# Performance work log

Hardware: AMD Instinct MI355X
Metric: run time of the kernel (lower is better)

## Reference

```python
import jax, jax.numpy as jnp
import numpy as np

B, L, D, H = 4, 1024, 1024, 16
DH = D // H
NEG = -1e9
EPS = 1e-5


def setup_inputs() -> dict:
    key = jax.random.key(0)
    ks = jax.random.split(key, 12)
    s = 1.0 / np.sqrt(D)
    inp = {
        "Q": jax.random.normal(ks[0], (B, L, D), jnp.float32),
        "K": jax.random.normal(ks[1], (B, L, D), jnp.float32),
        "V": jax.random.normal(ks[2], (B, L, D), jnp.float32),
        "K_mask": jnp.ones((B, L), jnp.int32),
        "WQ": jax.random.normal(ks[3], (D, D), jnp.float32) * s,
        "bQ": jnp.zeros((D,), jnp.float32),
        "WK": jax.random.normal(ks[4], (D, D), jnp.float32) * s,
        "bK": jnp.zeros((D,), jnp.float32),
        "WV": jax.random.normal(ks[5], (D, D), jnp.float32) * s,
        "bV": jnp.zeros((D,), jnp.float32),
        "WO": jax.random.normal(ks[6], (D, D), jnp.float32) * s,
        "bO": jnp.zeros((D,), jnp.float32),
        "ln_g": jnp.ones((D,), jnp.float32),
        "ln_b": jnp.zeros((D,), jnp.float32),
    }
    return inp


def _mha(Q, K, V, K_mask, WQ, bQ, WK, bK, WV, bV, WO, bO, ln_g, ln_b):
    # projections  [B,L,D]
    q = Q @ WQ + bQ
    k = K @ WK + bK
    v = V @ WV + bV
    # split heads -> [B,H,L,dh]
    q = q.reshape(B, L, H, DH).transpose(0, 2, 1, 3)
    k = k.reshape(B, L, H, DH).transpose(0, 2, 1, 3)
    v = v.reshape(B, L, H, DH).transpose(0, 2, 1, 3)
    # scaled dot product, masked softmax over keys
    scores = jnp.einsum("bhqd,bhkd->bhqk", q, k) / jnp.sqrt(jnp.float32(DH))
    mask = (K_mask > 0)[:, None, None, :]  # [B,1,1,Lk]
    scores = jnp.where(mask, scores, NEG)
    attn = jax.nn.softmax(scores, axis=-1)  # dropout is identity at inference
    ctx = jnp.einsum("bhqk,bhkd->bhqd", attn, v)
    ctx = ctx.transpose(0, 2, 1, 3).reshape(B, L, D)
    # output layer: dense + residual + layernorm
    out = ctx @ WO + bO
    x = out + Q
    mu = jnp.mean(x, axis=-1, keepdims=True)
    var = jnp.var(x, axis=-1, keepdims=True)
    return (x - mu) * jax.lax.rsqrt(var + EPS) * ln_g + ln_b


def reference(Q, K, V, K_mask, WQ, bQ, WK, bK, WV, bV, WO, bO, ln_g, ln_b):
    return _mha(Q, K, V, K_mask, WQ, bQ, WK, bK, WV, bV, WO, bO, ln_g, ln_b)
```

## Files before the change

kernel.cpp:

```cpp
#include <hip/hip_runtime.h>
#include <hip/hip_bf16.h>
#include <stdint.h>

#define Bn 4
#define Ln 1024
#define Dn 1024
#define Hn 16
#define DHn 64
#define Mn (Bn*Ln)

typedef __attribute__((ext_vector_type(8))) short short8v;
typedef __attribute__((ext_vector_type(4))) float floatx4;

__device__ __forceinline__ unsigned short f2b(float f){
  union { float f; unsigned u; } v; v.f = f;
  unsigned r = (v.u + 0x7FFFu + ((v.u >> 16) & 1u)) >> 16;
  return (unsigned short)r;
}
__device__ __forceinline__ unsigned short f2b_fast(float f){
  __hip_bfloat16 h = __float2bfloat16(f);
  return *reinterpret_cast<unsigned short*>(&h);
}
__device__ __forceinline__ float b2f(unsigned short u){
  union { unsigned u; float f; } v; v.u = (unsigned)u << 16; return v.f;
}

typedef const unsigned __attribute__((address_space(1)))* gas1_t;
typedef unsigned __attribute__((address_space(3)))* las3_t;
__device__ __forceinline__ void gload16(const void* g, void* l){
  __builtin_amdgcn_global_load_lds((gas1_t)(uintptr_t)g, (las3_t)(uintptr_t)l, 16, 0, 0);
}

__global__ __launch_bounds__(256) void prep_k(const float* __restrict__ W0,
    const float* __restrict__ W1, const float* __restrict__ W2,
    const float* __restrict__ W3, unsigned short* __restrict__ Wt0,
    unsigned short* __restrict__ Wt1, unsigned short* __restrict__ Wt2,
    unsigned short* __restrict__ Wt3, const float* __restrict__ x0,
    const float* __restrict__ x1, const float* __restrict__ x2,
    unsigned short* __restrict__ o0, unsigned short* __restrict__ o1,
    unsigned short* __restrict__ o2)
{
  __shared__ float tile[64][65];
  if (blockIdx.x < 1024){
    const int z = blockIdx.x >> 8, rem = blockIdx.x & 255;
    const float* W; unsigned short* Wt;
    switch (z){
      case 0: W = W0; Wt = Wt0; break;
      case 1: W = W1; Wt = Wt1; break;
      case 2: W = W2; Wt = Wt2; break;
      default: W = W3; Wt = Wt3; break;
    }
    const int nb = (rem & 15) * 64, kb = (rem >> 4) * 64;
    const int tx = threadIdx.x & 63, ty = threadIdx.x >> 6;
    #pragma unroll
    for (int r = 0; r < 64; r += 4)
      tile[r + ty][tx] = W[(size_t)(kb + r + ty) * 1024 + nb + tx];
    __syncthreads();
    #pragma unroll
    for (int r = 0; r < 64; r += 4)
      Wt[(size_t)(nb + r + ty) * 1024 + kb + tx] = f2b(tile[tx][r + ty]);
  } else {
    const int i = (blockIdx.x - 1024) * 256 + threadIdx.x;
    const int sel = i >> 20, idx = i & 0xFFFFF;
    const float* x = sel == 0 ? x0 : (sel == 1 ? x1 : x2);
    unsigned short* o = sel == 0 ? o0 : (sel == 1 ? o1 : o2);
    float4 v = reinterpret_cast<const float4*>(x)[idx];
    union { unsigned short u[4]; uint2 q; } p;
    p.u[0] = f2b(v.x); p.u[1] = f2b(v.y); p.u[2] = f2b(v.z); p.u[3] = f2b(v.w);
    reinterpret_cast<uint2*>(o)[idx] = p.q;
  }
}

template<int MODE>
__device__ __forceinline__ void gemm8_core(const unsigned short* __restrict__ Ab,
    const unsigned short* __restrict__ Btp, const float* __restrict__ bias,
    void* __restrict__ outp, float scale, unsigned short* lds, int nt, int mt)
{
  const int tid = threadIdx.x;
  const int lane = tid & 63, wave = tid >> 6;
  const int wr = wave >> 2, wc = wave & 3;
  const int lg = lane >> 4, lr = lane & 15;
  const int m0 = mt * 256, n0 = nt * 256;

  const unsigned short* gAb[2];
  const unsigned short* gBb[2];
  int ldso[2];
  #pragma unroll
  for (int i = 0; i < 2; i++){
    int c = tid + 512 * i;
    int g16 = c >> 6, lrr = c & 15, lgg = (c >> 4) & 3;
    int row = g16 * 16 + lrr;
    gAb[i] = Ab  + (size_t)(m0 + row) * 1024 + lgg * 8;
    gBb[i] = Btp + (size_t)(n0 + row) * 1024 + lgg * 8;
    ldso[i] = c * 8;
  }
  auto stageA = [&](int sg){
    unsigned short* slot = lds + (sg & 3) * 16384;
    const int kcol = (sg >> 1) * 64 + (sg & 1) * 32;
    #pragma unroll
    for (int i = 0; i < 2; i++) gload16(gAb[i] + kcol, &slot[ldso[i]]);
  };
  auto stageB = [&](int sg){
    unsigned short* slot = lds + (sg & 3) * 16384 + 8192;
    const int kcol = (sg >> 1) * 64 + (sg & 1) * 32;
    #pragma unroll
    for (int i = 0; i < 2; i++) gload16(gBb[i] + kcol, &slot[ldso[i]]);
  };

  floatx4 acc[8][4] = {};

  stageA(0); stageB(0); stageA(1); stageB(1); stageA(2); stageB(2);

  for (int t = 0; t < 16; t++){
    unsigned short* slot0 = lds + ((2 * t) & 3) * 16384;
    unsigned short* slot1 = lds + ((2 * t + 1) & 3) * 16384;
    short8v af[4], bf[4];
    if (t < 15) asm volatile("s_waitcnt vmcnt(8)" ::: "memory");
    else        asm volatile("s_waitcnt vmcnt(4)" ::: "memory");
    __builtin_amdgcn_s_barrier();
    __builtin_amdgcn_sched_barrier(0);
    if (t < 15) stageA(2 * t + 3);
    #pragma unroll
    for (int n = 0; n < 4; n++)
      bf[n] = *reinterpret_cast<const short8v*>(&slot0[8192 + ((wc * 4 + n) * 64 + lane) * 8]);
    #pragma unroll
    for (int i2 = 0; i2 < 4; i2++)
      af[i2] = *reinterpret_cast<const short8v*>(&slot0[((wr * 8 + i2) * 64 + lane) * 8]);
    __builtin_amdgcn_s_setprio(1);
    #pragma unroll
    for (int a = 0; a < 4; a++)
      #pragma unroll
      for (int n = 0; n < 4; n++)
        acc[a][n] = __builtin_amdgcn_mfma_f32_16x16x32_bf16(af[a], bf[n], acc[a][n], 0, 0, 0);
    __builtin_amdgcn_s_setprio(0);
    if (t < 15) stageB(2 * t + 3);
    #pragma unroll
    for (int i2 = 0; i2 < 4; i2++)
      af[i2] = *reinterpret_cast<const short8v*>(&slot0[((wr * 8 + 4 + i2) * 64 + lane) * 8]);
    __builtin_amdgcn_s_setprio(1);
    #pragma unroll
    for (int a = 0; a < 4; a++)
      #pragma unroll
      for (int n = 0; n < 4; n++)
        acc[4 + a][n] = __builtin_amdgcn_mfma_f32_16x16x32_bf16(af[a], bf[n], acc[4 + a][n], 0, 0, 0);
    __builtin_amdgcn_s_setprio(0);
    __builtin_amdgcn_sched_barrier(0);
    if (t < 15) asm volatile("s_waitcnt vmcnt(8)" ::: "memory");
    else        asm volatile("s_waitcnt vmcnt(0)" ::: "memory");
    __builtin_amdgcn_s_barrier();
    __builtin_amdgcn_sched_barrier(0);
    if (t < 14) stageA(2 * t + 4);
    #pragma unroll
    for (int n = 0; n < 4; n++)
      bf[n] = *reinterpret_cast<const short8v*>(&slot1[8192 + ((wc * 4 + n) * 64 + lane) * 8]);
    #pragma unroll
    for (int i2 = 0; i2 < 4; i2++)
      af[i2] = *reinterpret_cast<const short8v*>(&slot1[((wr * 8 + i2) * 64 + lane) * 8]);
    __builtin_amdgcn_s_setprio(1);
    #pragma unroll
    for (int a = 0; a < 4; a++)
      #pragma unroll
      for (int n = 0; n < 4; n++)
        acc[a][n] = __builtin_amdgcn_mfma_f32_16x16x32_bf16(af[a], bf[n], acc[a][n], 0, 0, 0);
    __builtin_amdgcn_s_setprio(0);
    if (t < 14) stageB(2 * t + 4);
    #pragma unroll
    for (int i2 = 0; i2 < 4; i2++)
      af[i2] = *reinterpret_cast<const short8v*>(&slot1[((wr * 8 + 4 + i2) * 64 + lane) * 8]);
    __builtin_amdgcn_s_setprio(1);
    #pragma unroll
    for (int a = 0; a < 4; a++)
      #pragma unroll
      for (int n = 0; n < 4; n++)
        acc[4 + a][n] = __builtin_amdgcn_mfma_f32_16x16x32_bf16(af[a], bf[n], acc[4 + a][n], 0, 0, 0);
    __builtin_amdgcn_s_setprio(0);
    __builtin_amdgcn_sched_barrier(0);
  }

  if constexpr (MODE == 2){
    __syncthreads();
    #pragma unroll
    for (int n = 0; n < 4; n++){
      const int gn_l = wc * 64 + n * 16 + lr;
      const float bb = bias[n0 + gn_l];
      const int X = (gn_l & 7) << 3;
      #pragma unroll
      for (int a = 0; a < 8; a++){
        const int gm_l = wr * 128 + a * 16 + lg * 4;
        union { unsigned short u[4]; uint2 q; } pk;
        #pragma unroll
        for (int r = 0; r < 4; r++) pk.u[r] = f2b((acc[a][n][r] + bb) * scale);
        *reinterpret_cast<uint2*>(&lds[gn_l * 256 + (gm_l ^ X)]) = pk.q;
      }
    }
    __syncthreads();
    const int bb2 = m0 >> 10, l0 = m0 & 1023;
    const int row = tid >> 1, colb = (tid & 1) * 128;
    const int h2 = (n0 + row) >> 6, d = (n0 + row) & 63;
    unsigned short* obase = (unsigned short*)outp +
        (((size_t)(bb2 * Hn + h2)) * DHn + d) * Ln + l0 + colb;
    const int XR = (row & 7) << 3;
    #pragma unroll
    for (int g = 0; g < 16; g++){
      short8v v = *reinterpret_cast<const short8v*>(&lds[row * 256 + ((colb + g * 8) ^ XR)]);
      *reinterpret_cast<short8v*>(obase + g * 8) = v;
    }
  } else {
    unsigned short* plw = lds + wave * 1152;
    unsigned short* o = (unsigned short*)outp;
    const int gnb = n0 + wc * 64;
    const int h2 = gnb >> 6;
    float bb4[4];
    #pragma unroll
    for (int n = 0; n < 4; n++) bb4[n] = bias[gnb + n * 16 + lr];
    #pragma unroll
    for (int a = 0; a < 8; a++){
      #pragma unroll
      for (int n = 0; n < 4; n++)
        #pragma unroll
        for (int r = 0; r < 4; r++)
          plw[(lg * 4 + r) * 72 + n * 16 + lr] = f2b((acc[a][n][r] + bb4[n]) * scale);
      #pragma unroll
      for (int it = 0; it < 2; it++){
        const int row = it * 8 + (lane >> 3);
        const int c   = lane & 7;
        const int gm  = m0 + wr * 128 + a * 16 + row;
        const int b2 = gm >> 10, l = gm & 1023;
        short8v v = *reinterpret_cast<const short8v*>(&plw[row * 72 + c * 8]);
        *reinterpret_cast<short8v*>(o + (((size_t)(b2 * Hn + h2)) * Ln + l) * DHn + c * 8) = v;
      }
    }
  }
}

__global__ __launch_bounds__(512, 2) void gemmqkv8_k(
    const unsigned short* __restrict__ A0, const unsigned short* __restrict__ A1,
    const unsigned short* __restrict__ A2, const unsigned short* __restrict__ W0,
    const unsigned short* __restrict__ W1, const unsigned short* __restrict__ W2,
    const float* __restrict__ b0, const float* __restrict__ b1,
    const float* __restrict__ b2, unsigned short* __restrict__ o0,
    unsigned short* __restrict__ o1, unsigned short* __restrict__ o2, float qscl)
{
  __shared__ __align__(16) unsigned short lds[65536];
  const int g = blockIdx.x >> 3;
  const int nt = g & 3;
  const int panel = (g >> 2) * 8 + (blockIdx.x & 7);
  const int z = panel >> 4, mt = panel & 15;
  if (z == 0)
    gemm8_core<0>(A0, W0, b0, o0, qscl, lds, nt, mt);
  else if (z == 1)
    gemm8_core<0>(A1, W1, b1, o1, 1.f, lds, nt, mt);
  else
    gemm8_core<2>(A2, W2, b2, o2, 1.f, lds, nt, mt);
}

__global__ __launch_bounds__(256) void gemmo_k(const unsigned short* __restrict__ Ab,
    const unsigned short* __restrict__ W, const float* __restrict__ bias,
    unsigned short* __restrict__ out, const float* __restrict__ resid)
{
  __shared__ __align__(16) unsigned short lds[32768];
  const int bid = blockIdx.x;
  const int xcd = bid & 7, k = bid >> 3;
  const int mt = xcd * 4 + (k >> 3);
  const int nt = k & 7;

  const int tid = threadIdx.x;
  const int lane = tid & 63, wave = tid >> 6;
  const int wr = wave >> 1, wc = wave & 1;
  const int lg = lane >> 4, lr = lane & 15;
  const int m0 = mt * 128, n0 = nt * 128;

  const unsigned short* gA[2];
  const unsigned short* gB[2];
  int ldso[2];
  #pragma unroll
  for (int i = 0; i < 2; i++){
    int c = tid + 256 * i;
    int g16 = c >> 6, lrr = c & 15, lgg = (c >> 4) & 3;
    int row = g16 * 16 + lrr;
    gA[i] = Ab + (size_t)(m0 + row) * 1024 + lgg * 8;
    gB[i] = W  + (size_t)(n0 + row) * 1024 + lgg * 8;
    ldso[i] = c * 8;
  }
  auto issue = [&](int s){
    unsigned short* base = lds + (s & 3) * 8192;
    const int kc = s * 32;
    #pragma unroll
    for (int i = 0; i < 2; i++) gload16(gA[i] + kc, &base[ldso[i]]);
    #pragma unroll
    for (int i = 0; i < 2; i++) gload16(gB[i] + kc, &base[4096 + ldso[i]]);
  };

  floatx4 acc[4][4] = {};

  issue(0); issue(1); issue(2);

  for (int s = 0; s < 32; s++){
    unsigned short* base = lds + (s & 3) * 8192;
    if (s <= 29)      asm volatile("s_waitcnt vmcnt(8)" ::: "memory");
    else if (s == 30) asm volatile("s_waitcnt vmcnt(4)" ::: "memory");
    else              asm volatile("s_waitcnt vmcnt(0)" ::: "memory");
    __builtin_amdgcn_s_barrier();
    __builtin_amdgcn_sched_barrier(0);
    if (s <= 28) issue(s + 3);
    short8v af[4], bf[4];
    #pragma unroll
    for (int m = 0; m < 4; m++)
      af[m] = *reinterpret_cast<const short8v*>(&base[((wr * 4 + m) * 64 + lane) * 8]);
    #pragma unroll
    for (int n = 0; n < 4; n++)
      bf[n] = *reinterpret_cast<const short8v*>(&base[4096 + ((wc * 4 + n) * 64 + lane) * 8]);
    __builtin_amdgcn_s_setprio(1);
    #pragma unroll
    for (int m = 0; m < 4; m++)
      #pragma unroll
      for (int n = 0; n < 4; n++)
        acc[m][n] = __builtin_amdgcn_mfma_f32_16x16x32_bf16(af[m], bf[n], acc[m][n], 0, 0, 0);
    __builtin_amdgcn_s_setprio(0);
    __builtin_amdgcn_sched_barrier(0);
  }

  unsigned short* plw = lds + wave * 1152;
  float bb4[4];
  #pragma unroll
  for (int n = 0; n < 4; n++) bb4[n] = bias[n0 + wc * 64 + n * 16 + lr];
  #pragma unroll
  for (int m = 0; m < 4; m++){
    #pragma unroll
    for (int n = 0; n < 4; n++){
      const int gn = n0 + wc * 64 + n * 16 + lr;
      #pragma unroll
      for (int r = 0; r < 4; r++){
        const int gm = m0 + wr * 64 + m * 16 + lg * 4 + r;
        float v = acc[m][n][r] + bb4[n] + resid[(size_t)gm * Dn + gn];
        plw[(lg * 4 + r) * 72 + n * 16 + lr] = f2b_fast(v);
      }
    }
    #pragma unroll
    for (int it = 0; it < 2; it++){
      const int row = it * 8 + (lane >> 3);
      const int c = lane & 7;
      const int gm = m0 + wr * 64 + m * 16 + row;
      short8v v = *reinterpret_cast<const short8v*>(&plw[row * 72 + c * 8]);
      *reinterpret_cast<short8v*>(out + (size_t)gm * Dn + n0 + wc * 64 + c * 8) = v;
    }
  }
}

__global__ __launch_bounds__(256) void attn_k(const unsigned short* __restrict__ qb,
    const unsigned short* __restrict__ kbf, const unsigned short* __restrict__ vtb,
    const int* __restrict__ kmask, unsigned short* __restrict__ ctx)
{
  const int bh = blockIdx.x;
  const int qt = blockIdx.y;
  const int b = bh >> 4, h = bh & 15;
  const int tid = threadIdx.x;
  const int w = tid >> 6, lane = tid & 63;
  const int lg = lane >> 4, lr = lane & 15;

  const unsigned short* qp = qb  + (size_t)bh * Ln * DHn;
  const unsigned short* kp = kbf + (size_t)bh * Ln * DHn;
  const unsigned short* vp = vtb + (size_t)bh * DHn * Ln;
  const int q0 = qt * 128 + w * 32;

  __shared__ __align__(16) unsigned short ldsK[3][4096];
  __shared__ __align__(16) unsigned short ldsV[3][4096];
  __shared__ __align__(16) unsigned short plds[4][32][72];
  __shared__ __align__(16) int ldsM[1024];

  short8v aq[2][2];
  #pragma unroll
  for (int f = 0; f < 2; f++)
    #pragma unroll
    for (int ks = 0; ks < 2; ks++)
      aq[f][ks] = *reinterpret_cast<const short8v*>(
          qp + (size_t)(q0 + f * 16 + lr) * DHn + ks * 32 + lg * 8);

  const unsigned short* gK[2];
  const unsigned short* gV[2];
  #pragma unroll
  for (int i = 0; i < 2; i++){
    int bc = w * 2 + i;
    int ks = bc >> 2, j = bc & 3;
    int row = j * 16 + lr, col = ks * 32 + lg * 8;
    gK[i] = kp + (size_t)row * DHn + col;
    gV[i] = vp + (size_t)row * Ln  + col;
  }
  auto issue = [&](int t){
    unsigned short* bK = ldsK[t % 3];
    unsigned short* bV = ldsV[t % 3];
    #pragma unroll
    for (int i = 0; i < 2; i++){
      gload16(gK[i] + (size_t)t * 4096, &bK[(w * 2 + i) * 512]);
      gload16(gV[i] + (size_t)t * 64,   &bV[(w * 2 + i) * 512]);
    }
  };

  floatx4 accO[2][4] = {};
  float lsacc[2][4] = {{0.f,0.f,0.f,0.f},{0.f,0.f,0.f,0.f}};

  gload16(kmask + b * Ln + w * 256 + lane * 4, &ldsM[w * 256]);
  issue(0);
  issue(1);

  for (int t = 0; t < 16; t++){
    if (t < 15) asm volatile("s_waitcnt vmcnt(4)" ::: "memory");
    else        asm volatile("s_waitcnt vmcnt(0)" ::: "memory");
    __builtin_amdgcn_s_barrier();
    __builtin_amdgcn_sched_barrier(0);
    if (t < 14) issue(t + 2);

    const unsigned short* bK = ldsK[t % 3];
    const unsigned short* bV = ldsV[t % 3];

    floatx4 s[2][4] = {};
    #pragma unroll
    for (int ks = 0; ks < 2; ks++)
      #pragma unroll
      for (int j = 0; j < 4; j++){
        short8v bk = *reinterpret_cast<const short8v*>(&bK[((ks * 4 + j) * 64 + lane) * 8]);
        s[0][j] = __builtin_amdgcn_mfma_f32_16x16x32_bf16(aq[0][ks], bk, s[0][j], 0, 0, 0);
        s[1][j] = __builtin_amdgcn_mfma_f32_16x16x32_bf16(aq[1][ks], bk, s[1][j], 0, 0, 0);
      }
    int mk[4];
    #pragma unroll
    for (int j = 0; j < 4; j++) mk[j] = ldsM[t * 64 + j * 16 + lr];
    if (__all(mk[0] > 0 && mk[1] > 0 && mk[2] > 0 && mk[3] > 0)){
      #pragma unroll
      for (int f = 0; f < 2; f++)
        #pragma unroll
        for (int j = 0; j < 4; j++)
          #pragma unroll
          for (int r = 0; r < 4; r++){
            float p = __builtin_amdgcn_exp2f(s[f][j][r]);
            lsacc[f][r] += p;
            plds[w][f * 16 + lg * 4 + r][j * 16 + lr] = f2b_fast(p);
          }
    } else {
      #pragma unroll
      for (int j = 0; j < 4; j++){
        const float madd = mk[j] > 0 ? 0.f : -1e9f;
        #pragma unroll
        for (int f = 0; f < 2; f++)
          #pragma unroll
          for (int r = 0; r < 4; r++){
            float p = __builtin_amdgcn_exp2f(s[f][j][r] + madd);
            lsacc[f][r] += p;
            plds[w][f * 16 + lg * 4 + r][j * 16 + lr] = f2b_fast(p);
          }
      }
    }
    #pragma unroll
    for (int ks = 0; ks < 2; ks++){
      short8v pa0 = *reinterpret_cast<const short8v*>(&plds[w][lr][ks * 32 + lg * 8]);
      short8v pa1 = *reinterpret_cast<const short8v*>(&plds[w][16 + lr][ks * 32 + lg * 8]);
      #pragma unroll
      for (int n = 0; n < 4; n++){
        short8v bv = *reinterpret_cast<const short8v*>(&bV[((ks * 4 + n) * 64 + lane) * 8]);
        accO[0][n] = __builtin_amdgcn_mfma_f32_16x16x32_bf16(pa0, bv, accO[0][n], 0, 0, 0);
        accO[1][n] = __builtin_amdgcn_mfma_f32_16x16x32_bf16(pa1, bv, accO[1][n], 0, 0, 0);
      }
    }
  }

  #pragma unroll
  for (int f = 0; f < 2; f++)
    #pragma unroll
    for (int r = 0; r < 4; r++){
      lsacc[f][r] += __shfl_xor(lsacc[f][r], 1, 64);
      lsacc[f][r] += __shfl_xor(lsacc[f][r], 2, 64);
      lsacc[f][r] += __shfl_xor(lsacc[f][r], 4, 64);
      lsacc[f][r] += __shfl_xor(lsacc[f][r], 8, 64);
      lsacc[f][r] = 1.f / fmaxf(lsacc[f][r], 1e-20f);
    }
  #pragma unroll
  for (int f = 0; f < 2; f++)
    #pragma unroll
    for (int n = 0; n < 4; n++)
      #pragma unroll
      for (int r = 0; r < 4; r++)
        plds[w][f * 16 + lg * 4 + r][n * 16 + lr] = f2b_fast(accO[f][n][r] * lsacc[f][r]);
  #pragma unroll
  for (int it = 0; it < 4; it++){
    const int row = it * 8 + (lane >> 3);
    const int c = lane & 7;
    const int q = q0 + row;
    short8v v = *reinterpret_cast<const short8v*>(&plds[w][row][c * 8]);
    *reinterpret_cast<short8v*>(ctx + ((size_t)(b * Ln + q)) * Dn + h * DHn + c * 8) = v;
  }
}

__global__ __launch_bounds__(256) void ln_k(const unsigned short* __restrict__ x,
    const float* __restrict__ g, const float* __restrict__ bt, float* __restrict__ out)
{
  const int row = blockIdx.x;
  const int tid = threadIdx.x;
  uint2 u = *reinterpret_cast<const uint2*>(x + (size_t)row * 1024 + tid * 4);
  float v0 = b2f((unsigned short)(u.x & 0xFFFF));
  float v1 = b2f((unsigned short)(u.x >> 16));
  float v2 = b2f((unsigned short)(u.y & 0xFFFF));
  float v3 = b2f((unsigned short)(u.y >> 16));
  float s  = v0 + v1 + v2 + v3;
  float sq = v0 * v0 + v1 * v1 + v2 * v2 + v3 * v3;
  #pragma unroll
  for (int off = 32; off >= 1; off >>= 1){
    s  += __shfl_xor(s, off, 64);
    sq += __shfl_xor(sq, off, 64);
  }
  __shared__ float psm[4], pqm[4];
  const int w = tid >> 6;
  if ((tid & 63) == 0){ psm[w] = s; pqm[w] = sq; }
  __syncthreads();
  s  = psm[0] + psm[1] + psm[2] + psm[3];
  sq = pqm[0] + pqm[1] + pqm[2] + pqm[3];
  const float mean = s * (1.f / 1024.f);
  const float var  = sq * (1.f / 1024.f) - mean * mean;
  const float inv  = rsqrtf(var + 1e-5f);
  float4 gg = *reinterpret_cast<const float4*>(g  + tid * 4);
  float4 bb = *reinterpret_cast<const float4*>(bt + tid * 4);
  float4 o;
  o.x = (v0 - mean) * inv * gg.x + bb.x;
  o.y = (v1 - mean) * inv * gg.y + bb.y;
  o.z = (v2 - mean) * inv * gg.z + bb.z;
  o.w = (v3 - mean) * inv * gg.w + bb.w;
  *reinterpret_cast<float4*>(out + (size_t)row * 1024 + tid * 4) = o;
}

extern "C" void kernel_launch(void* const* d_in, const int* in_sizes, int n_in,
                              void* d_out, int out_size, void* d_ws, size_t ws_size,
                              hipStream_t stream)
{
  const float* Qin = (const float*)d_in[0];
  const float* Kin = (const float*)d_in[1];
  const float* Vin = (const float*)d_in[2];
  const int*   Kms = (const int*)d_in[3];
  const float* WQ  = (const float*)d_in[4];
  const float* bQ  = (const float*)d_in[5];
  const float* WK  = (const float*)d_in[6];
  const float* bK  = (const float*)d_in[7];
  const float* WV  = (const float*)d_in[8];
  const float* bV  = (const float*)d_in[9];
  const float* WO  = (const float*)d_in[10];
  const float* bO  = (const float*)d_in[11];
  const float* lng = (const float*)d_in[12];
  const float* lnb = (const float*)d_in[13];

  char* ws = (char*)d_ws;
  const size_t MB = 1024u * 1024u;
  unsigned short* wqt = (unsigned short*)(ws + 0 * MB);
  unsigned short* wkt = (unsigned short*)(ws + 2 * MB);
  unsigned short* wvt = (unsigned short*)(ws + 4 * MB);
  unsigned short* wot = (unsigned short*)(ws + 6 * MB);
  unsigned short* qbf = (unsigned short*)(ws + 8 * MB);
  unsigned short* kbf = (unsigned short*)(ws + 16 * MB);
  unsigned short* vtb = (unsigned short*)(ws + 24 * MB);
  unsigned short* ctx = (unsigned short*)(ws + 32 * MB);
  unsigned short* xbh = (unsigned short*)(ws + 40 * MB);
  unsigned short* cv0 = (unsigned short*)(ws + 32 * MB);
  unsigned short* cv1 = (unsigned short*)(ws + 40 * MB);
  unsigned short* cv2 = (unsigned short*)(ws + 48 * MB);

  dim3 blk(256);
  prep_k<<<13312, blk, 0, stream>>>(WQ, WK, WV, WO, wqt, wkt, wvt, wot,
                                    Qin, Kin, Vin, cv0, cv1, cv2);

  const float QSCL = 0.125f * 1.44269504088896f;
  gemmqkv8_k<<<192, dim3(512), 0, stream>>>(cv0, cv1, cv2, wqt, wkt, wvt,
                                            bQ, bK, bV, qbf, kbf, vtb, QSCL);

  attn_k<<<dim3(64, 8), blk, 0, stream>>>(qbf, kbf, vtb, Kms, ctx);

  gemmo_k<<<256, blk, 0, stream>>>(ctx, wot, bO, xbh, Qin);

  ln_k<<<4096, blk, 0, stream>>>(xbh, lng, lnb, (float*)d_out);
}
```

Baseline: 117.4 us.

## Load QKV GEMM B operand directly from global into registers, halve LDS

```diff
diff --git a/kernel.cpp b/kernel.cpp
--- a/kernel.cpp
+++ b/kernel.cpp
@@ -83,46 +83,48 @@
   const int m0 = mt * 256, n0 = nt * 256;
 
   const unsigned short* gAb[2];
-  const unsigned short* gBb[2];
   int ldso[2];
   #pragma unroll
   for (int i = 0; i < 2; i++){
     int c = tid + 512 * i;
     int g16 = c >> 6, lrr = c & 15, lgg = (c >> 4) & 3;
-    int row = g16 * 16 + lrr;
-    gAb[i] = Ab  + (size_t)(m0 + row) * 1024 + lgg * 8;
-    gBb[i] = Btp + (size_t)(n0 + row) * 1024 + lgg * 8;
+    gAb[i] = Ab + (size_t)(m0 + g16 * 16 + lrr) * 1024 + lgg * 8;
     ldso[i] = c * 8;
   }
   auto stageA = [&](int sg){
-    unsigned short* slot = lds + (sg & 3) * 16384;
+    unsigned short* slot = lds + (sg & 3) * 8192;
     const int kcol = (sg >> 1) * 64 + (sg & 1) * 32;
     #pragma unroll
     for (int i = 0; i < 2; i++) gload16(gAb[i] + kcol, &slot[ldso[i]]);
   };
-  auto stageB = [&](int sg){
-    unsigned short* slot = lds + (sg & 3) * 16384 + 8192;
-    const int kcol = (sg >> 1) * 64 + (sg & 1) * 32;
-    #pragma unroll
-    for (int i = 0; i < 2; i++) gload16(gBb[i] + kcol, &slot[ldso[i]]);
+  const unsigned short* gBr[4];
+  #pragma unroll
+  for (int n = 0; n < 4; n++)
+    gBr[n] = Btp + (size_t)(n0 + wc * 64 + n * 16 + lr) * 1024 + lg * 8;
+  auto loadB = [&](int t, short8v (&Bs)[8]){
+    #pragma unroll
+    for (int ks = 0; ks < 2; ks++)
+      #pragma unroll
+      for (int n = 0; n < 4; n++)
+        Bs[ks * 4 + n] = *reinterpret_cast<const short8v*>(gBr[n] + t * 64 + ks * 32);
   };
 
   floatx4 acc[8][4] = {};
-
-  stageA(0); stageB(0); stageA(1); stageB(1); stageA(2); stageB(2);
-
-  for (int t = 0; t < 16; t++){
-    unsigned short* slot0 = lds + ((2 * t) & 3) * 16384;
-    unsigned short* slot1 = lds + ((2 * t + 1) & 3) * 16384;
-    short8v af[4], bf[4];
-    if (t < 15) asm volatile("s_waitcnt vmcnt(8)" ::: "memory");
-    else        asm volatile("s_waitcnt vmcnt(4)" ::: "memory");
+  short8v Bev[8], Bod[8];
+
+  stageA(0); stageA(1); stageA(2);
+  loadB(0, Bev); loadB(1, Bod);
+
+  auto tileStep = [&](int t, short8v (&Bc)[8]){
+    unsigned short* slot0 = lds + ((2 * t) & 3) * 8192;
+    unsigned short* slot1 = lds + ((2 * t + 1) & 3) * 8192;
+    short8v af[4];
+    if (t == 0)      asm volatile("s_waitcnt vmcnt(8)" ::: "memory");
+    else if (t < 15) asm volatile("s_waitcnt vmcnt(10)" ::: "memory");
+    else             asm volatile("s_waitcnt vmcnt(0)" ::: "memory");
     __builtin_amdgcn_s_barrier();
     __builtin_amdgcn_sched_barrier(0);
-    if (t < 15) stageA(2 * t + 3);
-    #pragma unroll
-    for (int n = 0; n < 4; n++)
-      bf[n] = *reinterpret_cast<const short8v*>(&slot0[8192 + ((wc * 4 + n) * 64 + lane) * 8]);
+    if (t <= 14) stageA(2 * t + 3);
     #pragma unroll
     for (int i2 = 0; i2 < 4; i2++)
       af[i2] = *reinterpret_cast<const short8v*>(&slot0[((wr * 8 + i2) * 64 + lane) * 8]);
@@ -131,9 +133,8 @@
     for (int a = 0; a < 4; a++)
       #pragma unroll
       for (int n = 0; n < 4; n++)
-        acc[a][n] = __builtin_amdgcn_mfma_f32_16x16x32_bf16(af[a], bf[n], acc[a][n], 0, 0, 0);
+        acc[a][n] = __builtin_amdgcn_mfma_f32_16x16x32_bf16(af[a], Bc[n], acc[a][n], 0, 0, 0);
     __builtin_amdgcn_s_setprio(0);
-    if (t < 15) stageB(2 * t + 3);
     #pragma unroll
     for (int i2 = 0; i2 < 4; i2++)
       af[i2] = *reinterpret_cast<const short8v*>(&slot0[((wr * 8 + 4 + i2) * 64 + lane) * 8]);
@@ -142,17 +143,12 @@
     for (int a = 0; a < 4; a++)
       #pragma unroll
       for (int n = 0; n < 4; n++)
-        acc[4 + a][n] = __builtin_amdgcn_mfma_f32_16x16x32_bf16(af[a], bf[n], acc[4 + a][n], 0, 0, 0);
+        acc[4 + a][n] = __builtin_amdgcn_mfma_f32_16x16x32_bf16(af[a], Bc[n], acc[4 + a][n], 0, 0, 0);
     __builtin_amdgcn_s_setprio(0);
     __builtin_amdgcn_sched_barrier(0);
-    if (t < 15) asm volatile("s_waitcnt vmcnt(8)" ::: "memory");
-    else        asm volatile("s_waitcnt vmcnt(0)" ::: "memory");
     __builtin_amdgcn_s_barrier();
     __builtin_amdgcn_sched_barrier(0);
-    if (t < 14) stageA(2 * t + 4);
-    #pragma unroll
-    for (int n = 0; n < 4; n++)
-      bf[n] = *reinterpret_cast<const short8v*>(&slot1[8192 + ((wc * 4 + n) * 64 + lane) * 8]);
+    if (t <= 13) stageA(2 * t + 4);
     #pragma unroll
     for (int i2 = 0; i2 < 4; i2++)
       af[i2] = *reinterpret_cast<const short8v*>(&slot1[((wr * 8 + i2) * 64 + lane) * 8]);
@@ -161,9 +157,8 @@
     for (int a = 0; a < 4; a++)
       #pragma unroll
       for (int n = 0; n < 4; n++)
-        acc[a][n] = __builtin_amdgcn_mfma_f32_16x16x32_bf16(af[a], bf[n], acc[a][n], 0, 0, 0);
+        acc[a][n] = __builtin_amdgcn_mfma_f32_16x16x32_bf16(af[a], Bc[4 + n], acc[a][n], 0, 0, 0);
     __builtin_amdgcn_s_setprio(0);
-    if (t < 14) stageB(2 * t + 4);
     #pragma unroll
     for (int i2 = 0; i2 < 4; i2++)
       af[i2] = *reinterpret_cast<const short8v*>(&slot1[((wr * 8 + 4 + i2) * 64 + lane) * 8]);
@@ -172,38 +167,51 @@
     for (int a = 0; a < 4; a++)
       #pragma unroll
       for (int n = 0; n < 4; n++)
-        acc[4 + a][n] = __builtin_amdgcn_mfma_f32_16x16x32_bf16(af[a], bf[n], acc[4 + a][n], 0, 0, 0);
+        acc[4 + a][n] = __builtin_amdgcn_mfma_f32_16x16x32_bf16(af[a], Bc[4 + n], acc[4 + a][n], 0, 0, 0);
     __builtin_amdgcn_s_setprio(0);
     __builtin_amdgcn_sched_barrier(0);
+    if (t <= 13) loadB(t + 2, Bc);
+    __builtin_amdgcn_sched_barrier(0);
+  };
+
+  for (int tt = 0; tt < 8; tt++){
+    tileStep(2 * tt,     Bev);
+    tileStep(2 * tt + 1, Bod);
   }
 
   if constexpr (MODE == 2){
-    __syncthreads();
-    #pragma unroll
-    for (int n = 0; n < 4; n++){
-      const int gn_l = wc * 64 + n * 16 + lr;
-      const float bb = bias[n0 + gn_l];
-      const int X = (gn_l & 7) << 3;
-      #pragma unroll
-      for (int a = 0; a < 8; a++){
-        const int gm_l = wr * 128 + a * 16 + lg * 4;
-        union { unsigned short u[4]; uint2 q; } pk;
+    #pragma unroll
+    for (int hp = 0; hp < 2; hp++){
+      __syncthreads();
+      if ((wc >> 1) == hp){
         #pragma unroll
-        for (int r = 0; r < 4; r++) pk.u[r] = f2b((acc[a][n][r] + bb) * scale);
-        *reinterpret_cast<uint2*>(&lds[gn_l * 256 + (gm_l ^ X)]) = pk.q;
-      }
-    }
-    __syncthreads();
-    const int bb2 = m0 >> 10, l0 = m0 & 1023;
-    const int row = tid >> 1, colb = (tid & 1) * 128;
-    const int h2 = (n0 + row) >> 6, d = (n0 + row) & 63;
-    unsigned short* obase = (unsigned short*)outp +
-        (((size_t)(bb2 * Hn + h2)) * DHn + d) * Ln + l0 + colb;
-    const int XR = (row & 7) << 3;
-    #pragma unroll
-    for (int g = 0; g < 16; g++){
-      short8v v = *reinterpret_cast<const short8v*>(&lds[row * 256 + ((colb + g * 8) ^ XR)]);
-      *reinterpret_cast<short8v*>(obase + g * 8) = v;
+        for (int n = 0; n < 4; n++){
+          const int grow = (wc & 1) * 64 + n * 16 + lr;
+          const float bb = bias[n0 + hp * 128 + grow];
+          const int X = (grow & 7) << 3;
+          #pragma unroll
+          for (int a = 0; a < 8; a++){
+            const int gm_l = wr * 128 + a * 16 + lg * 4;
+            union { unsigned short u[4]; uint2 q; } pk;
+            #pragma unroll
+            for (int r = 0; r < 4; r++) pk.u[r] = f2b((acc[a][n][r] + bb) * scale);
+            *reinterpret_cast<uint2*>(&lds[grow * 256 + (gm_l ^ X)]) = pk.q;
+          }
+        }
+      }
+      __syncthreads();
+      const int row_l = tid >> 2, colb = (tid & 3) * 64;
+      const int grow2 = n0 + hp * 128 + row_l;
+      const int h2 = grow2 >> 6, d = grow2 & 63;
+      const int bb2 = m0 >> 10, l0 = m0 & 1023;
+      unsigned short* obase = (unsigned short*)outp +
+          (((size_t)(bb2 * Hn + h2)) * DHn + d) * Ln + l0 + colb;
+      const int XR = (row_l & 7) << 3;
+      #pragma unroll
+      for (int g = 0; g < 8; g++){
+        short8v v = *reinterpret_cast<const short8v*>(&lds[row_l * 256 + ((colb + g * 8) ^ XR)]);
+        *reinterpret_cast<short8v*>(obase + g * 8) = v;
+      }
     }
   } else {
     unsigned short* plw = lds + wave * 1152;
@@ -241,7 +249,7 @@
     const float* __restrict__ b2, unsigned short* __restrict__ o0,
     unsigned short* __restrict__ o1, unsigned short* __restrict__ o2, float qscl)
 {
-  __shared__ __align__(16) unsigned short lds[65536];
+  __shared__ __align__(16) unsigned short lds[32768];
   const int g = blockIdx.x >> 3;
   const int nt = g & 3;
   const int panel = (g >> 2) * 8 + (blockIdx.x & 7);
```

New measurement: 142.8 us. 21.6% more time.
